# Kernel tuning notes

Hardware: AMD Instinct MI355X
Metric: run time of the kernel (lower is better)

The kernel has to match this reference:

```python
import jax, jax.numpy as jnp
import numpy as np

N = 50000      # nodes
E = 800000     # edges (avg degree 16)
F_IN = 128     # input features
H, C = 4, 16   # heads, per-head out channels -> conv out = 64
D = 128        # target_dim (proj output)
NEG_SLOPE = 0.2
LN_EPS = 1e-5


def setup_inputs() -> dict:
    key = jax.random.key(0)
    ks = jax.random.split(key, 8)
    s_in = 1.0 / np.sqrt(F_IN)
    s_hc = 1.0 / np.sqrt(H * C)
    return {
        "x": jax.random.normal(ks[0], (N, F_IN), jnp.float32),
        "edge_index": jax.random.randint(ks[1], (2, E), 0, N, jnp.int64),
        "W": jax.random.normal(ks[2], (F_IN, H * C), jnp.float32) * s_in,
        "att_src": jax.random.normal(ks[3], (H, C), jnp.float32) * s_hc,
        "att_dst": jax.random.normal(ks[4], (H, C), jnp.float32) * s_hc,
        "bias": jnp.zeros((H * C,), jnp.float32),
        "proj_w": jax.random.normal(ks[5], (D, H * C), jnp.float32) * s_hc,
        "proj_b": jnp.zeros((D,), jnp.float32),
        "gamma": jnp.ones((D,), jnp.float32),
        "beta": jnp.zeros((D,), jnp.float32),
    }


def reference(x, edge_index, W, att_src, att_dst, bias, proj_w, proj_b, gamma, beta):
    src, dst = edge_index[0], edge_index[1]
    # GATConv: per-head linear transform  [N, H, C]
    xp = (x @ W).reshape(N, H, C)
    a_src = jnp.einsum("nhc,hc->nh", xp, att_src)  # [N, H]
    a_dst = jnp.einsum("nhc,hc->nh", xp, att_dst)  # [N, H]
    # raw attention logits per edge, per head  [E, H]
    e = jax.nn.leaky_relu(a_src[src] + a_dst[dst], NEG_SLOPE)
    # segment softmax over incoming edges of each destination node
    m = jax.ops.segment_max(e, dst, num_segments=N)          # [N, H]
    ex = jnp.exp(e - m[dst])                                 # [E, H]
    denom = jax.ops.segment_sum(ex, dst, num_segments=N)     # [N, H]
    alpha = ex / (denom[dst] + 1e-16)                        # [E, H]
    # weighted message aggregation  [N, H, C]
    out = jax.ops.segment_sum(alpha[:, :, None] * xp[src], dst, num_segments=N)
    out = out.reshape(N, H * C) + bias                       # concat heads
    # projection to target_dim
    out = out @ proj_w.T + proj_b                            # [N, D]
    # LayerNorm over feature dim
    mu = out.mean(axis=-1, keepdims=True)
    var = out.var(axis=-1, keepdims=True)
    out = (out - mu) * jax.lax.rsqrt(var + LN_EPS) * gamma + beta
    # activation (relu); dropout=0.0 -> identity
    return jax.nn.relu(out)
```

## Files before the change

### kernel.cpp

```cpp
#include <hip/hip_runtime.h>
#include <hip/hip_bf16.h>


#define LEAKY(x) ((x) > 0.f ? (x) : 0.2f * (x))
#define CHUNK 2048
#define NBUK_PAD 256

typedef __attribute__((ext_vector_type(8))) short bf16x8;
typedef __attribute__((ext_vector_type(8))) unsigned short u16x8;
typedef __attribute__((ext_vector_type(4))) float f32x4;

static __device__ __forceinline__ unsigned short f2bf_rne(float f) {
    unsigned u = __float_as_uint(f);
    return (unsigned short)((u + 0x7FFFu + ((u >> 16) & 1u)) >> 16);
}
static __device__ __forceinline__ float bf2f(unsigned short h) {
    return __uint_as_float(((unsigned)h) << 16);
}

__global__ __launch_bounds__(256) void k_prep_part1(
    const float* __restrict__ W, const float* __restrict__ bias,
    const float* __restrict__ proj_w, const float* __restrict__ proj_b,
    unsigned short* __restrict__ Whf, unsigned short* __restrict__ Wlf,
    unsigned short* __restrict__ Phf, unsigned short* __restrict__ Plf,
    float* __restrict__ pb2,
    const int* __restrict__ dst, int* __restrict__ cnt, int E, int nchunk)
{
    int bid = blockIdx.x, t = threadIdx.x;
    if (bid < nchunk) {
        __shared__ int hist[NBUK_PAD];
        hist[t] = 0;
        __syncthreads();
        int e0 = bid * CHUNK;
#pragma unroll
        for (int i = 0; i < CHUNK / 256; i++) {
            int e = e0 + i * 256 + t;
            if (e < E) atomicAdd(&hist[dst[e] >> 8], 1);
        }
        __syncthreads();
        cnt[bid * NBUK_PAD + t] = hist[t];
        return;
    }
    int idx = (bid - nchunk) * 256 + t;
    if (idx < 8192) {
        int j = idx & 7, lane = (idx >> 3) & 63, ts = idx >> 9;
        int tt = ts >> 2, s = ts & 3;
        int k = s * 32 + ((lane >> 4) << 3) + j;
        int n = tt * 16 + (lane & 15);
        float w = W[k * 64 + n];
        unsigned short wh = f2bf_rne(w);
        Whf[idx] = wh;
        Wlf[idx] = f2bf_rne(w - bf2f(wh));
    } else if (idx < 16384) {
        int i2 = idx - 8192;
        int j = i2 & 7, lane = (i2 >> 3) & 63, ts = i2 >> 9;
        int tt = ts >> 1, s = ts & 1;
        int k = s * 32 + ((lane >> 4) << 3) + j;
        int d = tt * 16 + (lane & 15);
        float w = proj_w[d * 64 + k];
        unsigned short wh = f2bf_rne(w);
        Phf[i2] = wh;
        Plf[i2] = f2bf_rne(w - bf2f(wh));
    } else if (idx < 16384 + 128) {
        int d = idx - 16384;
        float s = proj_b[d];
        for (int j = 0; j < 64; j++) s += bias[j] * proj_w[d * 64 + j];
        pb2[d] = s;
    }
}

__global__ __launch_bounds__(256) void k_scanB1(int* __restrict__ cnt, int* __restrict__ bt,
                                                int nchunk)
{
    __shared__ int sh[256];
    int t = threadIdx.x, b = blockIdx.x;
    int v0 = (t < nchunk) ? cnt[t * NBUK_PAD + b] : 0;
    int v1 = (t + 256 < nchunk) ? cnt[(t + 256) * NBUK_PAD + b] : 0;
    sh[t] = v0; __syncthreads();
    for (int off = 1; off < 256; off <<= 1) {
        int u = (t >= off) ? sh[t - off] : 0;
        __syncthreads();
        sh[t] += u;
        __syncthreads();
    }
    int incl0 = sh[t], tot0 = sh[255];
    __syncthreads();
    sh[t] = v1; __syncthreads();
    for (int off = 1; off < 256; off <<= 1) {
        int u = (t >= off) ? sh[t - off] : 0;
        __syncthreads();
        sh[t] += u;
        __syncthreads();
    }
    int incl1 = sh[t] + tot0;
    if (t < nchunk) cnt[t * NBUK_PAD + b] = incl0 - v0;
    if (t + 256 < nchunk) cnt[(t + 256) * NBUK_PAD + b] = incl1 - v1;
    if (t == 255) bt[b] = incl1;
}

__global__ __launch_bounds__(256) void k_scanB2(const int* __restrict__ bt, int* __restrict__ bb,
                                                int* __restrict__ row_ptr, int n_nodes, int E)
{
    __shared__ int sh[256];
    int t = threadIdx.x;
    int v = bt[t];
    sh[t] = v; __syncthreads();
    for (int off = 1; off < 256; off <<= 1) {
        int u = (t >= off) ? sh[t - off] : 0;
        __syncthreads();
        sh[t] += u;
        __syncthreads();
    }
    bb[t] = sh[t] - v;
    if (t == 255) bb[256] = sh[255];
    if (t == 0) row_ptr[n_nodes] = E;
}

__global__ __launch_bounds__(256) void k_part2_xw(
    const int* __restrict__ src, const int* __restrict__ dst,
    const int* __restrict__ cnt, const int* __restrict__ bb,
    unsigned* __restrict__ part, int E,
    const float* __restrict__ x,
    const unsigned short* __restrict__ Whf, const unsigned short* __restrict__ Wlf,
    const float* __restrict__ att_src, const float* __restrict__ att_dst,
    unsigned short* __restrict__ xp, float* __restrict__ a_src, float* __restrict__ a_dst,
    int n_nodes, int P, int nbXw)
{
    __shared__ float xs[64][132];
    __shared__ int bases[NBUK_PAD];
    int bid = blockIdx.x, t = threadIdx.x;
    if (bid % P == P - 1) {
        int blk = bid / P;
        bases[t] = cnt[blk * NBUK_PAD + t] + bb[t];
        __syncthreads();
        int e0 = blk * CHUNK;
#pragma unroll
        for (int i = 0; i < CHUNK / 256; i++) {
            int e = e0 + i * 256 + t;
            if (e < E) {
                int d = dst[e];
                int s = src[e];
                int pos = atomicAdd(&bases[d >> 8], 1);
                part[pos] = ((unsigned)s << 8) | (unsigned)(d & 255);
            }
        }
        return;
    }
    int xb = bid - bid / P;
    if (xb >= nbXw) return;
    int xbase = xb * 64;
    for (int i = t; i < 64 * 32; i += 256) {
        int r = i >> 5, c = (i & 31) << 2;
        int gr = xbase + r; if (gr >= n_nodes) gr = n_nodes - 1;
        *(float4*)&xs[r][c] = *(const float4*)(x + (size_t)gr * 128 + c);
    }
    __syncthreads();
    int w = t >> 6, lane = t & 63;
    int mbase = xbase + w * 16;
    int mrow = lane & 15, kg = lane >> 4;
    int lrow = w * 16 + mrow;

    bf16x8 ah[4], al[4];
#pragma unroll
    for (int s = 0; s < 4; s++) {
        float4 v0 = *(const float4*)&xs[lrow][s * 32 + kg * 8];
        float4 v1 = *(const float4*)&xs[lrow][s * 32 + kg * 8 + 4];
        float f[8] = {v0.x, v0.y, v0.z, v0.w, v1.x, v1.y, v1.z, v1.w};
#pragma unroll
        for (int j = 0; j < 8; j++) {
            unsigned short h = f2bf_rne(f[j]);
            ah[s][j] = (short)h;
            al[s][j] = (short)f2bf_rne(f[j] - bf2f(h));
        }
    }

    f32x4 acc[4];
#pragma unroll
    for (int tt = 0; tt < 4; tt++) acc[tt] = (f32x4){0.f, 0.f, 0.f, 0.f};
#pragma unroll
    for (int tt = 0; tt < 4; tt++) {
#pragma unroll
        for (int s = 0; s < 4; s++) {
            size_t fi = (size_t)(((tt * 4 + s) * 64 + lane) * 8);
            bf16x8 bh = *(const bf16x8*)(Whf + fi);
            bf16x8 bl = *(const bf16x8*)(Wlf + fi);
            acc[tt] = __builtin_amdgcn_mfma_f32_16x16x32_bf16(ah[s], bh, acc[tt], 0, 0, 0);
            acc[tt] = __builtin_amdgcn_mfma_f32_16x16x32_bf16(ah[s], bl, acc[tt], 0, 0, 0);
            acc[tt] = __builtin_amdgcn_mfma_f32_16x16x32_bf16(al[s], bh, acc[tt], 0, 0, 0);
        }
    }

#pragma unroll
    for (int tt = 0; tt < 4; tt++) {
        float asv = att_src[tt * 16 + mrow];
        float adv = att_dst[tt * 16 + mrow];
#pragma unroll
        for (int r = 0; r < 4; r++) {
            float v = acc[tt][r];
            int n2 = mbase + kg * 4 + r;
            bool ok = (n2 < n_nodes);
            if (ok) xp[(size_t)n2 * 64 + tt * 16 + mrow] = f2bf_rne(v);
            float ts = v * asv;
            float td = v * adv;
#pragma unroll
            for (int off = 8; off; off >>= 1) {
                ts += __shfl_xor(ts, off);
                td += __shfl_xor(td, off);
            }
            if (mrow == 0 && ok) {
                a_src[n2 * 4 + tt] = ts;
                a_dst[n2 * 4 + tt] = td;
            }
        }
    }
}

__global__ __launch_bounds__(256) void k_csr(const unsigned* __restrict__ part, const int* __restrict__ bb,
                                             int* __restrict__ row_ptr, int* __restrict__ colsrc,
                                             int n_nodes)
{
    __shared__ int hist[256], off[256], sh[256];
    int t = threadIdx.x, b = blockIdx.x;
    int e0 = bb[b], e1 = bb[b + 1];
    int m = e1 - e0;
    hist[t] = 0;
    __syncthreads();
    for (int i = t; i < m; i += 256)
        atomicAdd(&hist[part[e0 + i] & 255u], 1);
    __syncthreads();
    int v = hist[t];
    sh[t] = v; __syncthreads();
    for (int o = 1; o < 256; o <<= 1) {
        int u = (t >= o) ? sh[t - o] : 0;
        __syncthreads();
        sh[t] += u;
        __syncthreads();
    }
    int excl = sh[t] - v;
    off[t] = excl;
    int node = b * 256 + t;
    if (node < n_nodes) row_ptr[node] = e0 + excl;
    __syncthreads();
    for (int i = t; i < m; i += 256) {
        unsigned u = part[e0 + i];
        int pos = atomicAdd(&off[u & 255u], 1);
        colsrc[e0 + pos] = (int)(u >> 8);
    }
}

__global__ __launch_bounds__(256, 8) void k_agg2(
    const unsigned short* __restrict__ xp, const float* __restrict__ a_src, const float* __restrict__ a_dst,
    const int* __restrict__ row_ptr, const int* __restrict__ colsrc,
    unsigned short* __restrict__ aggr, int n_nodes)
{
    __shared__ int   sstage[4][64];
    __shared__ float alpha_s[4][64][4];
    int t = threadIdx.x, w = t >> 6, lane = t & 63;
    int cgrp = lane & 7;
    int eoct = lane >> 3;
    int h = cgrp >> 1;
    int n = blockIdx.x * 4 + w;
    if (n >= n_nodes) return;
    int rp0 = row_ptr[n], rp1 = row_ptr[n + 1];
    float4 ad4 = *(const float4*)&a_dst[(size_t)n * 4];
    float acc[8] = {0.f, 0.f, 0.f, 0.f, 0.f, 0.f, 0.f, 0.f};
    float den = 0.f;
    for (int base = rp0; base < rp1; base += 64) {
        int cnt = rp1 - base; if (cnt > 64) cnt = 64;
        int s = 0;
        float4 p = make_float4(0.f, 0.f, 0.f, 0.f);
        if (lane < cnt) {
            s = colsrc[base + lane];
            float4 as4 = *(const float4*)&a_src[(size_t)s * 4];
            p.x = __expf(LEAKY(as4.x + ad4.x));
            p.y = __expf(LEAKY(as4.y + ad4.y));
            p.z = __expf(LEAKY(as4.z + ad4.z));
            p.w = __expf(LEAKY(as4.w + ad4.w));
        }
        sstage[w][lane] = s;
        *(float4*)&alpha_s[w][lane][0] = p;
        int iters = (cnt + 7) >> 3;
        for (int it = 0; it < iters; ++it) {
            int j = (it << 3) + eoct;
            int sj = sstage[w][j];
            float aj = alpha_s[w][j][h];
            u16x8 v = *(const u16x8*)(xp + (size_t)((unsigned)sj * 64u + (cgrp << 3)));
            den += aj;
#pragma unroll
            for (int q = 0; q < 8; q++) acc[q] += aj * bf2f(v[q]);
        }
    }
#pragma unroll
    for (int q = 0; q < 8; q++) {
        acc[q] += __shfl_xor(acc[q], 8);
        acc[q] += __shfl_xor(acc[q], 16);
        acc[q] += __shfl_xor(acc[q], 32);
    }
    den += __shfl_xor(den, 8);
    den += __shfl_xor(den, 16);
    den += __shfl_xor(den, 32);
    if (eoct == 0) {
        float inv = 1.f / (den + 1e-16f);
        u16x8 o;
#pragma unroll
        for (int q = 0; q < 8; q++) o[q] = f2bf_rne(acc[q] * inv);
        *(u16x8*)(aggr + (size_t)n * 64 + (cgrp << 3)) = o;
    }
}

__global__ __launch_bounds__(256, 4) void k_proj(
    const unsigned short* __restrict__ aggr,
    const unsigned short* __restrict__ Phf, const unsigned short* __restrict__ Plf,
    const float* __restrict__ pb2, const float* __restrict__ gamma, const float* __restrict__ beta,
    float* __restrict__ out, int n_nodes)
{
    __shared__ float pb_s[128], g_s[128], b_s[128];
    int t = threadIdx.x;
    if (t < 128) { pb_s[t] = pb2[t]; g_s[t] = gamma[t]; b_s[t] = beta[t]; }
    __syncthreads();
    int w = t >> 6, lane = t & 63;
    int mbase = blockIdx.x * 64 + w * 16;
    int mrow = lane & 15, kg = lane >> 4;
    int node = mbase + mrow;
    if (node >= n_nodes) node = n_nodes - 1;

    bf16x8 ah[2];
#pragma unroll
    for (int s = 0; s < 2; s++) {
        ah[s] = *(const bf16x8*)(aggr + (size_t)node * 64 + s * 32 + kg * 8);
    }

    f32x4 acc[8];
#pragma unroll
    for (int tt = 0; tt < 8; tt++) acc[tt] = (f32x4){0.f, 0.f, 0.f, 0.f};
#pragma unroll
    for (int tt = 0; tt < 8; tt++) {
#pragma unroll
        for (int s = 0; s < 2; s++) {
            size_t fi = (size_t)(((tt * 2 + s) * 64 + lane) * 8);
            bf16x8 bh = *(const bf16x8*)(Phf + fi);
            bf16x8 bl = *(const bf16x8*)(Plf + fi);
            acc[tt] = __builtin_amdgcn_mfma_f32_16x16x32_bf16(ah[s], bh, acc[tt], 0, 0, 0);
            acc[tt] = __builtin_amdgcn_mfma_f32_16x16x32_bf16(ah[s], bl, acc[tt], 0, 0, 0);
        }
    }

#pragma unroll
    for (int r = 0; r < 4; r++) {
        int nr = mbase + kg * 4 + r;
        float vv[8];
        float S = 0.f, Q = 0.f;
#pragma unroll
        for (int tt = 0; tt < 8; tt++) {
            float v = acc[tt][r] + pb_s[tt * 16 + mrow];
            vv[tt] = v;
            S += v;
            Q += v * v;
        }
#pragma unroll
        for (int off = 8; off; off >>= 1) {
            S += __shfl_xor(S, off);
            Q += __shfl_xor(Q, off);
        }
        float mu  = S * (1.f / 128.f);
        float var = Q * (1.f / 128.f) - mu * mu;
        float inv = rsqrtf(var + 1e-5f);
        if (nr < n_nodes) {
#pragma unroll
            for (int tt = 0; tt < 8; tt++) {
                int d = tt * 16 + mrow;
                float o = fmaxf((vv[tt] - mu) * inv * g_s[d] + b_s[d], 0.f);
                out[(size_t)nr * 128 + d] = o;
            }
        }
    }
}

extern "C" void kernel_launch(void* const* d_in, const int* in_sizes, int n_in,
                              void* d_out, int out_size, void* d_ws, size_t ws_size,
                              hipStream_t stream)
{
    const float* x       = (const float*)d_in[0];
    const int*   ei      = (const int*)  d_in[1];
    const float* W       = (const float*)d_in[2];
    const float* att_src = (const float*)d_in[3];
    const float* att_dst = (const float*)d_in[4];
    const float* bias    = (const float*)d_in[5];
    const float* proj_w  = (const float*)d_in[6];
    const float* proj_b  = (const float*)d_in[7];
    const float* gamma   = (const float*)d_in[8];
    const float* beta    = (const float*)d_in[9];

    int N = in_sizes[0] / 128;
    int E = in_sizes[1] / 2;
    const int* srcIdx = ei;
    const int* dstIdx = ei + E;

    int nchunk = (E + CHUNK - 1) / CHUNK;
    int NBUK   = (N + 255) / 256;
    int nbXw   = (N + 63) / 64;
    int nbPrep = (16512 + 255) / 256;

    char* ws = (char*)d_ws;
    unsigned short* xp   = (unsigned short*)ws; ws += (size_t)N * 64 * 2;
    unsigned short* aggr = (unsigned short*)ws; ws += (size_t)N * 64 * 2;
    float* a_src   = (float*)ws; ws += (size_t)N * 4 * 4;
    float* a_dst   = (float*)ws; ws += (size_t)N * 4 * 4;
    int*   row_ptr = (int*)ws;   ws += (size_t)(N + 1) * 4;
    int*   cnt     = (int*)ws;   ws += (size_t)nchunk * NBUK_PAD * 4;
    unsigned* part = (unsigned*)ws; ws += (size_t)E * 4;
    int*   colsrc  = (int*)ws;   ws += (size_t)E * 4;
    int*   bb      = (int*)ws;   ws += 257 * 4;
    int*   bt      = (int*)ws;   ws += 256 * 4;
    unsigned short* Whf = (unsigned short*)ws; ws += 8192 * 2;
    unsigned short* Wlf = (unsigned short*)ws; ws += 8192 * 2;
    unsigned short* Phf = (unsigned short*)ws; ws += 8192 * 2;
    unsigned short* Plf = (unsigned short*)ws; ws += 8192 * 2;
    float* pb2 = (float*)ws; ws += 128 * 4;

    int P = (nbXw + nchunk - 1) / nchunk + 1;
    int totalFused = nchunk * P;

    k_prep_part1<<<nchunk + nbPrep, 256, 0, stream>>>(W, bias, proj_w, proj_b,
                                                      Whf, Wlf, Phf, Plf, pb2,
                                                      dstIdx, cnt, E, nchunk);
    k_scanB1<<<256, 256, 0, stream>>>(cnt, bt, nchunk);
    k_scanB2<<<1, 256, 0, stream>>>(bt, bb, row_ptr, N, E);
    k_part2_xw<<<totalFused, 256, 0, stream>>>(srcIdx, dstIdx, cnt, bb, part, E,
                                               x, Whf, Wlf, att_src, att_dst,
                                               xp, a_src, a_dst, N, P, nbXw);
    k_csr<<<NBUK, 256, 0, stream>>>(part, bb, row_ptr, colsrc, N);
    k_agg2<<<(N + 3) / 4, 256, 0, stream>>>(xp, a_src, a_dst, row_ptr, colsrc, aggr, N);
    k_proj<<<(N + 63) / 64, 256, 0, stream>>>(aggr, Phf, Plf, pb2, gamma, beta, (float*)d_out, N);
}
```

Baseline: 85.72 us.

## Remove bucket-scan kernel by recomputing prefix in consumers; aggregate two nodes per wave

Drops the single-block k_scanB2 launch. The partition blocks and the CSR kernel each redo the 256-entry bucket-total scan locally, and the row_ptr end sentinel moves into scanB1. Separately, the aggregation kernel now handles two destination nodes per wavefront, interleaving their gathers to raise memory-level parallelism and halving the grid. The cost is redundant scan work, extra barriers in the partition blocks, more registers in the aggregation kernel, and divergence when the two nodes have different degrees.

```diff
diff --git a/kernel.cpp b/kernel.cpp
--- a/kernel.cpp
+++ b/kernel.cpp
@@ -70,7 +70,8 @@
 }
 
 __global__ __launch_bounds__(256) void k_scanB1(int* __restrict__ cnt, int* __restrict__ bt,
-                                                int nchunk)
+                                                int* __restrict__ row_ptr,
+                                                int nchunk, int n_nodes, int E)
 {
     __shared__ int sh[256];
     int t = threadIdx.x, b = blockIdx.x;
@@ -96,29 +97,12 @@
     if (t < nchunk) cnt[t * NBUK_PAD + b] = incl0 - v0;
     if (t + 256 < nchunk) cnt[(t + 256) * NBUK_PAD + b] = incl1 - v1;
     if (t == 255) bt[b] = incl1;
-}
-
-__global__ __launch_bounds__(256) void k_scanB2(const int* __restrict__ bt, int* __restrict__ bb,
-                                                int* __restrict__ row_ptr, int n_nodes, int E)
-{
-    __shared__ int sh[256];
-    int t = threadIdx.x;
-    int v = bt[t];
-    sh[t] = v; __syncthreads();
-    for (int off = 1; off < 256; off <<= 1) {
-        int u = (t >= off) ? sh[t - off] : 0;
-        __syncthreads();
-        sh[t] += u;
-        __syncthreads();
-    }
-    bb[t] = sh[t] - v;
-    if (t == 255) bb[256] = sh[255];
-    if (t == 0) row_ptr[n_nodes] = E;
+    if (b == 0 && t == 0) row_ptr[n_nodes] = E;
 }
 
 __global__ __launch_bounds__(256) void k_part2_xw(
     const int* __restrict__ src, const int* __restrict__ dst,
-    const int* __restrict__ cnt, const int* __restrict__ bb,
+    const int* __restrict__ cnt, const int* __restrict__ bt,
     unsigned* __restrict__ part, int E,
     const float* __restrict__ x,
     const unsigned short* __restrict__ Whf, const unsigned short* __restrict__ Wlf,
@@ -128,10 +112,19 @@
 {
     __shared__ float xs[64][132];
     __shared__ int bases[NBUK_PAD];
+    __shared__ int sh[256];
     int bid = blockIdx.x, t = threadIdx.x;
     if (bid % P == P - 1) {
         int blk = bid / P;
-        bases[t] = cnt[blk * NBUK_PAD + t] + bb[t];
+        int v = bt[t];
+        sh[t] = v; __syncthreads();
+        for (int off = 1; off < 256; off <<= 1) {
+            int u = (t >= off) ? sh[t - off] : 0;
+            __syncthreads();
+            sh[t] += u;
+            __syncthreads();
+        }
+        bases[t] = cnt[blk * NBUK_PAD + t] + (sh[t] - v);
         __syncthreads();
         int e0 = blk * CHUNK;
 #pragma unroll
@@ -215,20 +208,13 @@
     }
 }
 
-__global__ __launch_bounds__(256) void k_csr(const unsigned* __restrict__ part, const int* __restrict__ bb,
+__global__ __launch_bounds__(256) void k_csr(const unsigned* __restrict__ part, const int* __restrict__ bt,
                                              int* __restrict__ row_ptr, int* __restrict__ colsrc,
                                              int n_nodes)
 {
     __shared__ int hist[256], off[256], sh[256];
     int t = threadIdx.x, b = blockIdx.x;
-    int e0 = bb[b], e1 = bb[b + 1];
-    int m = e1 - e0;
-    hist[t] = 0;
-    __syncthreads();
-    for (int i = t; i < m; i += 256)
-        atomicAdd(&hist[part[e0 + i] & 255u], 1);
-    __syncthreads();
-    int v = hist[t];
+    int v = bt[t];
     sh[t] = v; __syncthreads();
     for (int o = 1; o < 256; o <<= 1) {
         int u = (t >= o) ? sh[t - o] : 0;
@@ -236,7 +222,24 @@
         sh[t] += u;
         __syncthreads();
     }
-    int excl = sh[t] - v;
+    int e0 = (b > 0) ? sh[b - 1] : 0;
+    int e1 = sh[b];
+    __syncthreads();
+    int m = e1 - e0;
+    hist[t] = 0;
+    __syncthreads();
+    for (int i = t; i < m; i += 256)
+        atomicAdd(&hist[part[e0 + i] & 255u], 1);
+    __syncthreads();
+    int hv = hist[t];
+    sh[t] = hv; __syncthreads();
+    for (int o = 1; o < 256; o <<= 1) {
+        int u = (t >= o) ? sh[t - o] : 0;
+        __syncthreads();
+        sh[t] += u;
+        __syncthreads();
+    }
+    int excl = sh[t] - hv;
     off[t] = excl;
     int node = b * 256 + t;
     if (node < n_nodes) row_ptr[node] = e0 + excl;
@@ -253,58 +256,119 @@
     const int* __restrict__ row_ptr, const int* __restrict__ colsrc,
     unsigned short* __restrict__ aggr, int n_nodes)
 {
-    __shared__ int   sstage[4][64];
-    __shared__ float alpha_s[4][64][4];
+    __shared__ int   sstage[4][2][64];
+    __shared__ float alpha_s[4][2][64][4];
     int t = threadIdx.x, w = t >> 6, lane = t & 63;
     int cgrp = lane & 7;
     int eoct = lane >> 3;
     int h = cgrp >> 1;
-    int n = blockIdx.x * 4 + w;
-    if (n >= n_nodes) return;
-    int rp0 = row_ptr[n], rp1 = row_ptr[n + 1];
-    float4 ad4 = *(const float4*)&a_dst[(size_t)n * 4];
-    float acc[8] = {0.f, 0.f, 0.f, 0.f, 0.f, 0.f, 0.f, 0.f};
-    float den = 0.f;
-    for (int base = rp0; base < rp1; base += 64) {
-        int cnt = rp1 - base; if (cnt > 64) cnt = 64;
-        int s = 0;
-        float4 p = make_float4(0.f, 0.f, 0.f, 0.f);
-        if (lane < cnt) {
-            s = colsrc[base + lane];
-            float4 as4 = *(const float4*)&a_src[(size_t)s * 4];
-            p.x = __expf(LEAKY(as4.x + ad4.x));
-            p.y = __expf(LEAKY(as4.y + ad4.y));
-            p.z = __expf(LEAKY(as4.z + ad4.z));
-            p.w = __expf(LEAKY(as4.w + ad4.w));
-        }
-        sstage[w][lane] = s;
-        *(float4*)&alpha_s[w][lane][0] = p;
-        int iters = (cnt + 7) >> 3;
+    int n0 = blockIdx.x * 8 + w * 2;
+    int n1 = n0 + 1;
+    if (n0 >= n_nodes) return;
+    bool has1 = (n1 < n_nodes);
+    int ra0 = row_ptr[n0], ra1 = row_ptr[n0 + 1];
+    int rb0 = has1 ? row_ptr[n1] : 0;
+    int rb1 = has1 ? row_ptr[n1 + 1] : 0;
+    float4 adA = *(const float4*)&a_dst[(size_t)n0 * 4];
+    float4 adB = adA;
+    if (has1) adB = *(const float4*)&a_dst[(size_t)n1 * 4];
+    float accA[8] = {0.f,0.f,0.f,0.f,0.f,0.f,0.f,0.f};
+    float accB[8] = {0.f,0.f,0.f,0.f,0.f,0.f,0.f,0.f};
+    float denA = 0.f, denB = 0.f;
+    int degA = ra1 - ra0, degB = rb1 - rb0;
+    int nb = ((degA > degB ? degA : degB) + 63) >> 6;
+    for (int b = 0; b < nb; ++b) {
+        int cA = degA - (b << 6); if (cA > 64) cA = 64;
+        int cB = degB - (b << 6); if (cB > 64) cB = 64;
+        {
+            int s = 0; float4 p = make_float4(0.f, 0.f, 0.f, 0.f);
+            if (lane < cA) {
+                s = colsrc[ra0 + (b << 6) + lane];
+                float4 as4 = *(const float4*)&a_src[(size_t)s * 4];
+                p.x = __expf(LEAKY(as4.x + adA.x));
+                p.y = __expf(LEAKY(as4.y + adA.y));
+                p.z = __expf(LEAKY(as4.z + adA.z));
+                p.w = __expf(LEAKY(as4.w + adA.w));
+            }
+            sstage[w][0][lane] = s;
+            *(float4*)&alpha_s[w][0][lane][0] = p;
+        }
+        {
+            int s = 0; float4 p = make_float4(0.f, 0.f, 0.f, 0.f);
+            if (lane < cB) {
+                s = colsrc[rb0 + (b << 6) + lane];
+                float4 as4 = *(const float4*)&a_src[(size_t)s * 4];
+                p.x = __expf(LEAKY(as4.x + adB.x));
+                p.y = __expf(LEAKY(as4.y + adB.y));
+                p.z = __expf(LEAKY(as4.z + adB.z));
+                p.w = __expf(LEAKY(as4.w + adB.w));
+            }
+            sstage[w][1][lane] = s;
+            *(float4*)&alpha_s[w][1][lane][0] = p;
+        }
+        int itA = cA > 0 ? ((cA + 7) >> 3) : 0;
+        int itB = cB > 0 ? ((cB + 7) >> 3) : 0;
+        int iters = itA > itB ? itA : itB;
         for (int it = 0; it < iters; ++it) {
             int j = (it << 3) + eoct;
-            int sj = sstage[w][j];
-            float aj = alpha_s[w][j][h];
-            u16x8 v = *(const u16x8*)(xp + (size_t)((unsigned)sj * 64u + (cgrp << 3)));
-            den += aj;
-#pragma unroll
-            for (int q = 0; q < 8; q++) acc[q] += aj * bf2f(v[q]);
+            u16x8 vA, vB;
+            float ajA = 0.f, ajB = 0.f;
+            bool dA = it < itA, dB = it < itB;
+            if (dA) {
+                int sj = sstage[w][0][j];
+                ajA = alpha_s[w][0][j][h];
+                vA = *(const u16x8*)(xp + (size_t)((unsigned)sj * 64u + (cgrp << 3)));
+            }
+            if (dB) {
+                int sj = sstage[w][1][j];
+                ajB = alpha_s[w][1][j][h];
+                vB = *(const u16x8*)(xp + (size_t)((unsigned)sj * 64u + (cgrp << 3)));
+            }
+            if (dA) {
+                denA += ajA;
+#pragma unroll
+                for (int q = 0; q < 8; q++) accA[q] += ajA * bf2f(vA[q]);
+            }
+            if (dB) {
+                denB += ajB;
+#pragma unroll
+                for (int q = 0; q < 8; q++) accB[q] += ajB * bf2f(vB[q]);
+            }
         }
     }
 #pragma unroll
     for (int q = 0; q < 8; q++) {
-        acc[q] += __shfl_xor(acc[q], 8);
-        acc[q] += __shfl_xor(acc[q], 16);
-        acc[q] += __shfl_xor(acc[q], 32);
-    }
-    den += __shfl_xor(den, 8);
-    den += __shfl_xor(den, 16);
-    den += __shfl_xor(den, 32);
+        accA[q] += __shfl_xor(accA[q], 8);
+        accA[q] += __shfl_xor(accA[q], 16);
+        accA[q] += __shfl_xor(accA[q], 32);
+    }
+    denA += __shfl_xor(denA, 8);
+    denA += __shfl_xor(denA, 16);
+    denA += __shfl_xor(denA, 32);
     if (eoct == 0) {
-        float inv = 1.f / (den + 1e-16f);
+        float inv = 1.f / (denA + 1e-16f);
         u16x8 o;
 #pragma unroll
-        for (int q = 0; q < 8; q++) o[q] = f2bf_rne(acc[q] * inv);
-        *(u16x8*)(aggr + (size_t)n * 64 + (cgrp << 3)) = o;
+        for (int q = 0; q < 8; q++) o[q] = f2bf_rne(accA[q] * inv);
+        *(u16x8*)(aggr + (size_t)n0 * 64 + (cgrp << 3)) = o;
+    }
+    if (has1) {
+#pragma unroll
+        for (int q = 0; q < 8; q++) {
+            accB[q] += __shfl_xor(accB[q], 8);
+            accB[q] += __shfl_xor(accB[q], 16);
+            accB[q] += __shfl_xor(accB[q], 32);
+        }
+        denB += __shfl_xor(denB, 8);
+        denB += __shfl_xor(denB, 16);
+        denB += __shfl_xor(denB, 32);
+        if (eoct == 0) {
+            float inv = 1.f / (denB + 1e-16f);
+            u16x8 o;
+#pragma unroll
+            for (int q = 0; q < 8; q++) o[q] = f2bf_rne(accB[q] * inv);
+            *(u16x8*)(aggr + (size_t)n1 * 64 + (cgrp << 3)) = o;
+        }
     }
 }
 
@@ -410,7 +474,6 @@
     int*   cnt     = (int*)ws;   ws += (size_t)nchunk * NBUK_PAD * 4;
     unsigned* part = (unsigned*)ws; ws += (size_t)E * 4;
     int*   colsrc  = (int*)ws;   ws += (size_t)E * 4;
-    int*   bb      = (int*)ws;   ws += 257 * 4;
     int*   bt      = (int*)ws;   ws += 256 * 4;
     unsigned short* Whf = (unsigned short*)ws; ws += 8192 * 2;
     unsigned short* Wlf = (unsigned short*)ws; ws += 8192 * 2;
@@ -424,12 +487,11 @@
     k_prep_part1<<<nchunk + nbPrep, 256, 0, stream>>>(W, bias, proj_w, proj_b,
                                                       Whf, Wlf, Phf, Plf, pb2,
                                                       dstIdx, cnt, E, nchunk);
-    k_scanB1<<<256, 256, 0, stream>>>(cnt, bt, nchunk);
-    k_scanB2<<<1, 256, 0, stream>>>(bt, bb, row_ptr, N, E);
-    k_part2_xw<<<totalFused, 256, 0, stream>>>(srcIdx, dstIdx, cnt, bb, part, E,
+    k_scanB1<<<256, 256, 0, stream>>>(cnt, bt, row_ptr, nchunk, N, E);
+    k_part2_xw<<<totalFused, 256, 0, stream>>>(srcIdx, dstIdx, cnt, bt, part, E,
                                                x, Whf, Wlf, att_src, att_dst,
                                                xp, a_src, a_dst, N, P, nbXw);
-    k_csr<<<NBUK, 256, 0, stream>>>(part, bb, row_ptr, colsrc, N);
-    k_agg2<<<(N + 3) / 4, 256, 0, stream>>>(xp, a_src, a_dst, row_ptr, colsrc, aggr, N);
+    k_csr<<<NBUK, 256, 0, stream>>>(part, bt, row_ptr, colsrc, N);
+    k_agg2<<<(N + 7) / 8, 256, 0, stream>>>(xp, a_src, a_dst, row_ptr, colsrc, aggr, N);
     k_proj<<<(N + 63) / 64, 256, 0, stream>>>(aggr, Phf, Plf, pb2, gamma, beta, (float*)d_out, N);
 }
```

After: 89.89 us. +4.9%, slower.

## Fuse aggregation with projection+LayerNorm and fold single-block scan into consumers

Applied to the files above, without the earlier changes.

Removes the k_scanB2 launch by redundantly recomputing the bucket-total scan inside k_part2_xw's partition blocks and inside k_csr. Fuses the per-node attention aggregation with the MFMA projection and LayerNorm. Each block now aggregates 16 nodes into a shared-memory row buffer, then its 4 waves each compute 2 of the 8 output tiles and combine LayerNorm statistics through shared memory. This drops the bf16 aggr round trip through global memory and one launch. The cost is fewer, larger blocks (16 nodes per block instead of 4), lower occupancy via launch bounds, extra block barriers, and redundant scan work.

```diff
diff --git a/kernel.cpp b/kernel.cpp
--- a/kernel.cpp
+++ b/kernel.cpp
@@ -70,7 +70,8 @@
 }
 
 __global__ __launch_bounds__(256) void k_scanB1(int* __restrict__ cnt, int* __restrict__ bt,
-                                                int nchunk)
+                                                int* __restrict__ row_ptr,
+                                                int nchunk, int n_nodes, int E)
 {
     __shared__ int sh[256];
     int t = threadIdx.x, b = blockIdx.x;
@@ -96,29 +97,12 @@
     if (t < nchunk) cnt[t * NBUK_PAD + b] = incl0 - v0;
     if (t + 256 < nchunk) cnt[(t + 256) * NBUK_PAD + b] = incl1 - v1;
     if (t == 255) bt[b] = incl1;
-}
-
-__global__ __launch_bounds__(256) void k_scanB2(const int* __restrict__ bt, int* __restrict__ bb,
-                                                int* __restrict__ row_ptr, int n_nodes, int E)
-{
-    __shared__ int sh[256];
-    int t = threadIdx.x;
-    int v = bt[t];
-    sh[t] = v; __syncthreads();
-    for (int off = 1; off < 256; off <<= 1) {
-        int u = (t >= off) ? sh[t - off] : 0;
-        __syncthreads();
-        sh[t] += u;
-        __syncthreads();
-    }
-    bb[t] = sh[t] - v;
-    if (t == 255) bb[256] = sh[255];
-    if (t == 0) row_ptr[n_nodes] = E;
+    if (b == 0 && t == 0) row_ptr[n_nodes] = E;
 }
 
 __global__ __launch_bounds__(256) void k_part2_xw(
     const int* __restrict__ src, const int* __restrict__ dst,
-    const int* __restrict__ cnt, const int* __restrict__ bb,
+    const int* __restrict__ cnt, const int* __restrict__ bt,
     unsigned* __restrict__ part, int E,
     const float* __restrict__ x,
     const unsigned short* __restrict__ Whf, const unsigned short* __restrict__ Wlf,
@@ -128,10 +112,19 @@
 {
     __shared__ float xs[64][132];
     __shared__ int bases[NBUK_PAD];
+    __shared__ int sh[256];
     int bid = blockIdx.x, t = threadIdx.x;
     if (bid % P == P - 1) {
         int blk = bid / P;
-        bases[t] = cnt[blk * NBUK_PAD + t] + bb[t];
+        int v = bt[t];
+        sh[t] = v; __syncthreads();
+        for (int off = 1; off < 256; off <<= 1) {
+            int u = (t >= off) ? sh[t - off] : 0;
+            __syncthreads();
+            sh[t] += u;
+            __syncthreads();
+        }
+        bases[t] = cnt[blk * NBUK_PAD + t] + (sh[t] - v);
         __syncthreads();
         int e0 = blk * CHUNK;
 #pragma unroll
@@ -215,20 +208,13 @@
     }
 }
 
-__global__ __launch_bounds__(256) void k_csr(const unsigned* __restrict__ part, const int* __restrict__ bb,
+__global__ __launch_bounds__(256) void k_csr(const unsigned* __restrict__ part, const int* __restrict__ bt,
                                              int* __restrict__ row_ptr, int* __restrict__ colsrc,
                                              int n_nodes)
 {
     __shared__ int hist[256], off[256], sh[256];
     int t = threadIdx.x, b = blockIdx.x;
-    int e0 = bb[b], e1 = bb[b + 1];
-    int m = e1 - e0;
-    hist[t] = 0;
-    __syncthreads();
-    for (int i = t; i < m; i += 256)
-        atomicAdd(&hist[part[e0 + i] & 255u], 1);
-    __syncthreads();
-    int v = hist[t];
+    int v = bt[t];
     sh[t] = v; __syncthreads();
     for (int o = 1; o < 256; o <<= 1) {
         int u = (t >= o) ? sh[t - o] : 0;
@@ -236,7 +222,24 @@
         sh[t] += u;
         __syncthreads();
     }
-    int excl = sh[t] - v;
+    int e0 = (b > 0) ? sh[b - 1] : 0;
+    int e1 = sh[b];
+    __syncthreads();
+    int m = e1 - e0;
+    hist[t] = 0;
+    __syncthreads();
+    for (int i = t; i < m; i += 256)
+        atomicAdd(&hist[part[e0 + i] & 255u], 1);
+    __syncthreads();
+    int hv = hist[t];
+    sh[t] = hv; __syncthreads();
+    for (int o = 1; o < 256; o <<= 1) {
+        int u = (t >= o) ? sh[t - o] : 0;
+        __syncthreads();
+        sh[t] += u;
+        __syncthreads();
+    }
+    int excl = sh[t] - hv;
     off[t] = excl;
     int node = b * 256 + t;
     if (node < n_nodes) row_ptr[node] = e0 + excl;
@@ -248,112 +251,108 @@
     }
 }
 
-__global__ __launch_bounds__(256, 8) void k_agg2(
+__global__ __launch_bounds__(256, 6) void k_agg_proj(
     const unsigned short* __restrict__ xp, const float* __restrict__ a_src, const float* __restrict__ a_dst,
     const int* __restrict__ row_ptr, const int* __restrict__ colsrc,
-    unsigned short* __restrict__ aggr, int n_nodes)
+    const unsigned short* __restrict__ Phf, const unsigned short* __restrict__ Plf,
+    const float* __restrict__ pb2, const float* __restrict__ gamma, const float* __restrict__ beta,
+    float* __restrict__ out, int n_nodes)
 {
     __shared__ int   sstage[4][64];
     __shared__ float alpha_s[4][64][4];
+    __shared__ unsigned short rowbuf[16][72];
+    __shared__ float pS[4][16], pQ[4][16];
+    __shared__ float pb_s[128], g_s[128], b_s[128];
     int t = threadIdx.x, w = t >> 6, lane = t & 63;
+    if (t < 128) { pb_s[t] = pb2[t]; g_s[t] = gamma[t]; b_s[t] = beta[t]; }
     int cgrp = lane & 7;
     int eoct = lane >> 3;
     int h = cgrp >> 1;
-    int n = blockIdx.x * 4 + w;
-    if (n >= n_nodes) return;
-    int rp0 = row_ptr[n], rp1 = row_ptr[n + 1];
-    float4 ad4 = *(const float4*)&a_dst[(size_t)n * 4];
-    float acc[8] = {0.f, 0.f, 0.f, 0.f, 0.f, 0.f, 0.f, 0.f};
-    float den = 0.f;
-    for (int base = rp0; base < rp1; base += 64) {
-        int cnt = rp1 - base; if (cnt > 64) cnt = 64;
-        int s = 0;
-        float4 p = make_float4(0.f, 0.f, 0.f, 0.f);
-        if (lane < cnt) {
-            s = colsrc[base + lane];
-            float4 as4 = *(const float4*)&a_src[(size_t)s * 4];
-            p.x = __expf(LEAKY(as4.x + ad4.x));
-            p.y = __expf(LEAKY(as4.y + ad4.y));
-            p.z = __expf(LEAKY(as4.z + ad4.z));
-            p.w = __expf(LEAKY(as4.w + ad4.w));
-        }
-        sstage[w][lane] = s;
-        *(float4*)&alpha_s[w][lane][0] = p;
-        int iters = (cnt + 7) >> 3;
-        for (int it = 0; it < iters; ++it) {
-            int j = (it << 3) + eoct;
-            int sj = sstage[w][j];
-            float aj = alpha_s[w][j][h];
-            u16x8 v = *(const u16x8*)(xp + (size_t)((unsigned)sj * 64u + (cgrp << 3)));
-            den += aj;
-#pragma unroll
-            for (int q = 0; q < 8; q++) acc[q] += aj * bf2f(v[q]);
-        }
-    }
-#pragma unroll
-    for (int q = 0; q < 8; q++) {
-        acc[q] += __shfl_xor(acc[q], 8);
-        acc[q] += __shfl_xor(acc[q], 16);
-        acc[q] += __shfl_xor(acc[q], 32);
-    }
-    den += __shfl_xor(den, 8);
-    den += __shfl_xor(den, 16);
-    den += __shfl_xor(den, 32);
-    if (eoct == 0) {
-        float inv = 1.f / (den + 1e-16f);
-        u16x8 o;
-#pragma unroll
-        for (int q = 0; q < 8; q++) o[q] = f2bf_rne(acc[q] * inv);
-        *(u16x8*)(aggr + (size_t)n * 64 + (cgrp << 3)) = o;
-    }
-}
-
-__global__ __launch_bounds__(256, 4) void k_proj(
-    const unsigned short* __restrict__ aggr,
-    const unsigned short* __restrict__ Phf, const unsigned short* __restrict__ Plf,
-    const float* __restrict__ pb2, const float* __restrict__ gamma, const float* __restrict__ beta,
-    float* __restrict__ out, int n_nodes)
-{
-    __shared__ float pb_s[128], g_s[128], b_s[128];
-    int t = threadIdx.x;
-    if (t < 128) { pb_s[t] = pb2[t]; g_s[t] = gamma[t]; b_s[t] = beta[t]; }
-    __syncthreads();
-    int w = t >> 6, lane = t & 63;
-    int mbase = blockIdx.x * 64 + w * 16;
+    int nb16 = blockIdx.x * 16;
+
+    for (int i = 0; i < 4; i++) {
+        int n = nb16 + w * 4 + i;
+        int nl = w * 4 + i;
+        float acc[8] = {0.f,0.f,0.f,0.f,0.f,0.f,0.f,0.f};
+        float den = 0.f;
+        if (n < n_nodes) {
+            int rp0 = row_ptr[n], rp1 = row_ptr[n + 1];
+            float4 ad4 = *(const float4*)&a_dst[(size_t)n * 4];
+            for (int base = rp0; base < rp1; base += 64) {
+                int cnt = rp1 - base; if (cnt > 64) cnt = 64;
+                int s = 0;
+                float4 p = make_float4(0.f, 0.f, 0.f, 0.f);
+                if (lane < cnt) {
+                    s = colsrc[base + lane];
+                    float4 as4 = *(const float4*)&a_src[(size_t)s * 4];
+                    p.x = __expf(LEAKY(as4.x + ad4.x));
+                    p.y = __expf(LEAKY(as4.y + ad4.y));
+                    p.z = __expf(LEAKY(as4.z + ad4.z));
+                    p.w = __expf(LEAKY(as4.w + ad4.w));
+                }
+                sstage[w][lane] = s;
+                *(float4*)&alpha_s[w][lane][0] = p;
+                int iters = (cnt + 7) >> 3;
+                for (int it = 0; it < iters; ++it) {
+                    int j = (it << 3) + eoct;
+                    int sj = sstage[w][j];
+                    float aj = alpha_s[w][j][h];
+                    u16x8 v = *(const u16x8*)(xp + (size_t)((unsigned)sj * 64u + (cgrp << 3)));
+                    den += aj;
+#pragma unroll
+                    for (int q = 0; q < 8; q++) acc[q] += aj * bf2f(v[q]);
+                }
+            }
+#pragma unroll
+            for (int q = 0; q < 8; q++) {
+                acc[q] += __shfl_xor(acc[q], 8);
+                acc[q] += __shfl_xor(acc[q], 16);
+                acc[q] += __shfl_xor(acc[q], 32);
+            }
+            den += __shfl_xor(den, 8);
+            den += __shfl_xor(den, 16);
+            den += __shfl_xor(den, 32);
+        }
+        if (eoct == 0) {
+            float inv = 1.f / (den + 1e-16f);
+            u16x8 o;
+#pragma unroll
+            for (int q = 0; q < 8; q++) o[q] = f2bf_rne(acc[q] * inv);
+            *(u16x8*)&rowbuf[nl][cgrp << 3] = o;
+        }
+    }
+    __syncthreads();
+
     int mrow = lane & 15, kg = lane >> 4;
-    int node = mbase + mrow;
-    if (node >= n_nodes) node = n_nodes - 1;
-
     bf16x8 ah[2];
 #pragma unroll
     for (int s = 0; s < 2; s++) {
-        ah[s] = *(const bf16x8*)(aggr + (size_t)node * 64 + s * 32 + kg * 8);
-    }
-
-    f32x4 acc[8];
-#pragma unroll
-    for (int tt = 0; tt < 8; tt++) acc[tt] = (f32x4){0.f, 0.f, 0.f, 0.f};
-#pragma unroll
-    for (int tt = 0; tt < 8; tt++) {
+        ah[s] = *(const bf16x8*)&rowbuf[mrow][s * 32 + kg * 8];
+    }
+    f32x4 acc2[2];
+#pragma unroll
+    for (int ttl = 0; ttl < 2; ttl++) acc2[ttl] = (f32x4){0.f, 0.f, 0.f, 0.f};
+#pragma unroll
+    for (int ttl = 0; ttl < 2; ttl++) {
+        int tt = w * 2 + ttl;
 #pragma unroll
         for (int s = 0; s < 2; s++) {
             size_t fi = (size_t)(((tt * 2 + s) * 64 + lane) * 8);
             bf16x8 bh = *(const bf16x8*)(Phf + fi);
             bf16x8 bl = *(const bf16x8*)(Plf + fi);
-            acc[tt] = __builtin_amdgcn_mfma_f32_16x16x32_bf16(ah[s], bh, acc[tt], 0, 0, 0);
-            acc[tt] = __builtin_amdgcn_mfma_f32_16x16x32_bf16(ah[s], bl, acc[tt], 0, 0, 0);
-        }
-    }
-
+            acc2[ttl] = __builtin_amdgcn_mfma_f32_16x16x32_bf16(ah[s], bh, acc2[ttl], 0, 0, 0);
+            acc2[ttl] = __builtin_amdgcn_mfma_f32_16x16x32_bf16(ah[s], bl, acc2[ttl], 0, 0, 0);
+        }
+    }
+    float vv[2][4];
 #pragma unroll
     for (int r = 0; r < 4; r++) {
-        int nr = mbase + kg * 4 + r;
-        float vv[8];
         float S = 0.f, Q = 0.f;
 #pragma unroll
-        for (int tt = 0; tt < 8; tt++) {
-            float v = acc[tt][r] + pb_s[tt * 16 + mrow];
-            vv[tt] = v;
+        for (int ttl = 0; ttl < 2; ttl++) {
+            int tt = w * 2 + ttl;
+            float v = acc2[ttl][r] + pb_s[tt * 16 + mrow];
+            vv[ttl][r] = v;
             S += v;
             Q += v * v;
         }
@@ -362,14 +361,23 @@
             S += __shfl_xor(S, off);
             Q += __shfl_xor(Q, off);
         }
+        if (mrow == 0) { pS[w][kg * 4 + r] = S; pQ[w][kg * 4 + r] = Q; }
+    }
+    __syncthreads();
+#pragma unroll
+    for (int r = 0; r < 4; r++) {
+        int nl = kg * 4 + r;
+        int nr = nb16 + nl;
+        float S = pS[0][nl] + pS[1][nl] + pS[2][nl] + pS[3][nl];
+        float Q = pQ[0][nl] + pQ[1][nl] + pQ[2][nl] + pQ[3][nl];
         float mu  = S * (1.f / 128.f);
         float var = Q * (1.f / 128.f) - mu * mu;
         float inv = rsqrtf(var + 1e-5f);
         if (nr < n_nodes) {
 #pragma unroll
-            for (int tt = 0; tt < 8; tt++) {
-                int d = tt * 16 + mrow;
-                float o = fmaxf((vv[tt] - mu) * inv * g_s[d] + b_s[d], 0.f);
+            for (int ttl = 0; ttl < 2; ttl++) {
+                int d = (w * 2 + ttl) * 16 + mrow;
+                float o = fmaxf((vv[ttl][r] - mu) * inv * g_s[d] + b_s[d], 0.f);
                 out[(size_t)nr * 128 + d] = o;
             }
         }
@@ -402,15 +410,13 @@
     int nbPrep = (16512 + 255) / 256;
 
     char* ws = (char*)d_ws;
-    unsigned short* xp   = (unsigned short*)ws; ws += (size_t)N * 64 * 2;
-    unsigned short* aggr = (unsigned short*)ws; ws += (size_t)N * 64 * 2;
+    unsigned short* xp = (unsigned short*)ws; ws += (size_t)N * 64 * 2;
     float* a_src   = (float*)ws; ws += (size_t)N * 4 * 4;
     float* a_dst   = (float*)ws; ws += (size_t)N * 4 * 4;
     int*   row_ptr = (int*)ws;   ws += (size_t)(N + 1) * 4;
     int*   cnt     = (int*)ws;   ws += (size_t)nchunk * NBUK_PAD * 4;
     unsigned* part = (unsigned*)ws; ws += (size_t)E * 4;
     int*   colsrc  = (int*)ws;   ws += (size_t)E * 4;
-    int*   bb      = (int*)ws;   ws += 257 * 4;
     int*   bt      = (int*)ws;   ws += 256 * 4;
     unsigned short* Whf = (unsigned short*)ws; ws += 8192 * 2;
     unsigned short* Wlf = (unsigned short*)ws; ws += 8192 * 2;
@@ -424,12 +430,12 @@
     k_prep_part1<<<nchunk + nbPrep, 256, 0, stream>>>(W, bias, proj_w, proj_b,
                                                       Whf, Wlf, Phf, Plf, pb2,
                                                       dstIdx, cnt, E, nchunk);
-    k_scanB1<<<256, 256, 0, stream>>>(cnt, bt, nchunk);
-    k_scanB2<<<1, 256, 0, stream>>>(bt, bb, row_ptr, N, E);
-    k_part2_xw<<<totalFused, 256, 0, stream>>>(srcIdx, dstIdx, cnt, bb, part, E,
+    k_scanB1<<<256, 256, 0, stream>>>(cnt, bt, row_ptr, nchunk, N, E);
+    k_part2_xw<<<totalFused, 256, 0, stream>>>(srcIdx, dstIdx, cnt, bt, part, E,
                                                x, Whf, Wlf, att_src, att_dst,
                                                xp, a_src, a_dst, N, P, nbXw);
-    k_csr<<<NBUK, 256, 0, stream>>>(part, bb, row_ptr, colsrc, N);
-    k_agg2<<<(N + 3) / 4, 256, 0, stream>>>(xp, a_src, a_dst, row_ptr, colsrc, aggr, N);
-    k_proj<<<(N + 63) / 64, 256, 0, stream>>>(aggr, Phf, Plf, pb2, gamma, beta, (float*)d_out, N);
-}
+    k_csr<<<NBUK, 256, 0, stream>>>(part, bt, row_ptr, colsrc, N);
+    k_agg_proj<<<(N + 15) / 16, 256, 0, stream>>>(xp, a_src, a_dst, row_ptr, colsrc,
+                                                  Phf, Plf, pb2, gamma, beta,
+                                                  (float*)d_out, N);
+}
```

Measured after the change: 83.52 us. -2.6%, faster.
